# Kernel optimization log

Measured on AMD Instinct MI355X. Metric: run time of the kernel, lower is better.

Reference implementation:

```python
import jax, jax.numpy as jnp
import numpy as np

EMB = 384
H = 6
D = 64  # head_size = EMB // H
FF = 4 * EMB
B, T = 256, 256
EPS = 1e-5


def layernorm(x, g, b):
    mu = jnp.mean(x, axis=-1, keepdims=True)
    var = jnp.var(x, axis=-1, keepdims=True)
    return (x - mu) * jax.lax.rsqrt(var + EPS) * g + b


def setup_inputs() -> dict:
    key = jax.random.key(0)
    ks = jax.random.split(key, 12)
    s_qkv = 1.0 / np.sqrt(EMB)
    return {
        "x":  jax.random.normal(ks[0], (B, T, EMB), jnp.float32),
        # per-head Q/K/V projections stacked: [EMB, H, D]
        "Wq": jax.random.normal(ks[1], (EMB, H, D), jnp.float32) * s_qkv,
        "Wk": jax.random.normal(ks[2], (EMB, H, D), jnp.float32) * s_qkv,
        "Wv": jax.random.normal(ks[3], (EMB, H, D), jnp.float32) * s_qkv,
        "Wo": jax.random.normal(ks[4], (EMB, EMB), jnp.float32) * s_qkv,
        "bo": jnp.zeros((EMB,), jnp.float32),
        "W1": jax.random.normal(ks[5], (EMB, FF), jnp.float32) * s_qkv,
        "b1": jnp.zeros((FF,), jnp.float32),
        "W2": jax.random.normal(ks[6], (FF, EMB), jnp.float32) * (1.0 / np.sqrt(FF)),
        "b2": jnp.zeros((EMB,), jnp.float32),
        "g1": jnp.ones((EMB,), jnp.float32),
        "be1": jnp.zeros((EMB,), jnp.float32),
        "g2": jnp.ones((EMB,), jnp.float32),
        "be2": jnp.zeros((EMB,), jnp.float32),
    }


def reference(x, Wq, Wk, Wv, Wo, bo, W1, b1, W2, b2, g1, be1, g2, be2):
    # pre-LN attention (unmasked encoder block, dropout in eval mode = identity)
    h = layernorm(x, g1, be1)                      # [B,T,C]
    q = jnp.einsum('btc,chd->bhtd', h, Wq)
    k = jnp.einsum('btc,chd->bhtd', h, Wk)
    v = jnp.einsum('btc,chd->bhtd', h, Wv)
    scores = jnp.einsum('bhtd,bhsd->bhts', q, k) * (D ** -0.5)
    attn = jax.nn.softmax(scores, axis=-1)         # [B,H,T,T]
    o = jnp.einsum('bhts,bhsd->bhtd', attn, v)
    o = o.transpose(0, 2, 1, 3).reshape(x.shape[0], x.shape[1], EMB)  # concat heads
    x = x + o @ Wo + bo
    h2 = layernorm(x, g2, be2)
    ff = jax.nn.relu(h2 @ W1 + b1) @ W2 + b2
    return x + ff
```

## Files before the change

### kernel.cpp

```cpp
#include <hip/hip_runtime.h>

typedef __attribute__((ext_vector_type(8))) short bf16x8;
typedef __attribute__((ext_vector_type(4))) float f32x4;
typedef __attribute__((ext_vector_type(4))) unsigned short u16x4;

#define DEVFN static __device__ __forceinline__

DEVFN unsigned short f2b(float f) {
  union { float f; unsigned u; } x; x.f = f;
  unsigned r = x.u + 0x7FFFu + ((x.u >> 16) & 1u);
  return (unsigned short)(r >> 16);
}

DEVFN void gll16(const void* g, void* l) {
  __builtin_amdgcn_global_load_lds(
      (const __attribute__((address_space(1))) unsigned int*)g,
      (__attribute__((address_space(3))) unsigned int*)l, 16, 0, 0);
}

#define MFMA16(a, b, c) __builtin_amdgcn_mfma_f32_16x16x32_bf16((a), (b), (c), 0, 0, 0)

__global__ __launch_bounds__(256) void prep_kernel(
    const float* __restrict__ Wq, const float* __restrict__ Wk, const float* __restrict__ Wv,
    const float* __restrict__ Wo, const float* __restrict__ W1, const float* __restrict__ W2,
    short* __restrict__ wqkvT, short* __restrict__ woT,
    short* __restrict__ w1T, short* __restrict__ w2T)
{
  int idx = blockIdx.x * 256 + threadIdx.x;
  if (idx < 442368) {
    int n = idx / 384, kk = idx - n * 384;
    int sec = n / 384, ww = n - sec * 384;
    const float* s = sec == 0 ? Wq : (sec == 1 ? Wk : Wv);
    wqkvT[idx] = (short)f2b(s[kk * 384 + ww]);
  } else if (idx < 589824) {
    int j = idx - 442368;
    int n = j / 384, kk = j - n * 384;
    woT[j] = (short)f2b(Wo[kk * 384 + n]);
  } else if (idx < 1179648) {
    int j = idx - 589824;
    int n = j / 384, kk = j - n * 384;
    w1T[j] = (short)f2b(W1[kk * 1536 + n]);
  } else if (idx < 1769472) {
    int j = idx - 1179648;
    int n = j / 1536, kk = j - n * 1536;
    w2T[j] = (short)f2b(W2[kk * 384 + n]);
  }
}

__global__ __launch_bounds__(256) void ln_kernel(
    const float* __restrict__ x, const float* __restrict__ g, const float* __restrict__ b,
    short* __restrict__ out)
{
  int row = blockIdx.x * 4 + (threadIdx.x >> 6);
  int l = threadIdx.x & 63;
  const float* xr = x + (size_t)row * 384;
  float v[6], s = 0.f, s2 = 0.f;
  #pragma unroll
  for (int i = 0; i < 6; ++i) { v[i] = xr[l + 64 * i]; s += v[i]; s2 += v[i] * v[i]; }
  #pragma unroll
  for (int m = 1; m < 64; m <<= 1) { s += __shfl_xor(s, m); s2 += __shfl_xor(s2, m); }
  float mu = s * (1.f / 384.f);
  float rs = rsqrtf(s2 * (1.f / 384.f) - mu * mu + 1e-5f);
  short* orow = out + (size_t)row * 384;
  #pragma unroll
  for (int i = 0; i < 6; ++i) {
    int c = l + 64 * i;
    orow[c] = (short)f2b((v[i] - mu) * rs * g[c] + b[c]);
  }
}

template<int EPI>
__global__ __launch_bounds__(256) void gemm_bt(
    const short* __restrict__ A, const short* __restrict__ BT,
    int K, int kt, int N,
    const float* __restrict__ bias, const float* __restrict__ resid,
    float* __restrict__ fout, short* __restrict__ bout,
    short* __restrict__ qb, short* __restrict__ kb, short* __restrict__ vb)
{
  __shared__ short As[128 * 64];
  __shared__ short Bs[128 * 64];
  const int tid = threadIdx.x;
  const int l = tid & 63, w = tid >> 6;
  const int cl = l & 15, rq = l >> 4;
  const int wr = (w >> 1) * 64, wc = (w & 1) * 64;
  const int m0 = blockIdx.y * 128, n0 = blockIdx.x * 128;
  const short* Ab = A + (size_t)m0 * K;
  const short* Bb = BT + (size_t)n0 * K;

  f32x4 acc[4][4] = {};

  for (int ks = 0; ks < kt; ++ks) {
    const int k0 = ks * 64;
    __syncthreads();
    #pragma unroll
    for (int i = 0; i < 4; ++i) {
      int slot = i * 256 + tid;
      int row = slot >> 3, g = slot & 7;
      int gs = g ^ (row & 7);
      gll16(Ab + (size_t)row * K + k0 + gs * 8, &As[slot * 8]);
      gll16(Bb + (size_t)row * K + k0 + gs * 8, &Bs[slot * 8]);
    }
    __syncthreads();
    #pragma unroll
    for (int kk = 0; kk < 2; ++kk) {
      bf16x8 af[4], bfr[4];
      #pragma unroll
      for (int m = 0; m < 4; ++m) {
        int row = wr + m * 16 + cl;
        af[m] = *(const bf16x8*)&As[row * 64 + (((kk * 4 + rq) ^ (row & 7)) * 8)];
      }
      #pragma unroll
      for (int n = 0; n < 4; ++n) {
        int row = wc + n * 16 + cl;
        bfr[n] = *(const bf16x8*)&Bs[row * 64 + (((kk * 4 + rq) ^ (row & 7)) * 8)];
      }
      #pragma unroll
      for (int m = 0; m < 4; ++m)
        #pragma unroll
        for (int n = 0; n < 4; ++n)
          acc[m][n] = MFMA16(af[m], bfr[n], acc[m][n]);
    }
  }

  const int gr0 = m0 + wr, gc0 = n0 + wc;
  #pragma unroll
  for (int m = 0; m < 4; ++m) {
    #pragma unroll
    for (int n = 0; n < 4; ++n) {
      int col = gc0 + n * 16 + cl;
      int rbase = gr0 + m * 16 + rq * 4;
      if constexpr (EPI == 0) {
        int sec = col / 384;
        int wcol = col - sec * 384;
        int hh = wcol >> 6, d = wcol & 63;
        int bidx = rbase >> 8, t0 = rbase & 255;
        if (sec == 2) {
          u16x4 pk;
          #pragma unroll
          for (int r = 0; r < 4; ++r) pk[r] = f2b(acc[m][n][r]);
          *(u16x4*)&vb[((size_t)(bidx * 6 + hh) * 64 + d) * 256 + t0] = pk;
        } else {
          short* dst = (sec == 0) ? qb : kb;
          float sc = (sec == 0) ? 0.125f : 1.0f;
          #pragma unroll
          for (int r = 0; r < 4; ++r)
            dst[((size_t)(bidx * 6 + hh) * 256 + t0 + r) * 64 + d] = (short)f2b(acc[m][n][r] * sc);
        }
      } else if constexpr (EPI == 1) {
        #pragma unroll
        for (int r = 0; r < 4; ++r) {
          size_t ix = (size_t)(rbase + r) * N + col;
          fout[ix] = acc[m][n][r] + bias[col] + resid[ix];
        }
      } else {
        #pragma unroll
        for (int r = 0; r < 4; ++r)
          bout[(size_t)(rbase + r) * N + col] = (short)f2b(fmaxf(acc[m][n][r] + bias[col], 0.f));
      }
    }
  }
}

__global__ __launch_bounds__(256) void attn_kernel(
    const short* __restrict__ qg, const short* __restrict__ kg,
    const short* __restrict__ vg, short* __restrict__ og)
{
  __shared__ short Ks[256 * 64];
  __shared__ short Vs[64 * 256];
  __shared__ float Pb[4][16 * 36];
  const int tid = threadIdx.x;
  const int bh = blockIdx.x >> 2;
  const int q0 = (blockIdx.x & 3) * 64;
  const int w = tid >> 6, l = tid & 63;
  const int cl = l & 15, rq = l >> 4;
  const short* kgb = kg + (size_t)bh * 16384;
  const short* vgb = vg + (size_t)bh * 16384;
  #pragma unroll
  for (int i = 0; i < 8; ++i) {
    int slot = i * 256 + tid;
    int row = slot >> 3, g = slot & 7;
    gll16(kgb + row * 64 + (g ^ (row & 7)) * 8, &Ks[slot * 8]);
  }
  #pragma unroll
  for (int i = 0; i < 8; ++i) {
    int slot = i * 256 + tid;
    int row = slot >> 5, g = slot & 31;
    int gs = (g & 24) | ((g ^ row) & 7);
    gll16(vgb + row * 256 + gs * 8, &Vs[slot * 8]);
  }
  const int qrow = q0 + w * 16 + cl;
  const bf16x8* qp = (const bf16x8*)(qg + ((size_t)bh * 256 + qrow) * 64 + rq * 8);
  bf16x8 qf0 = qp[0];
  bf16x8 qf1 = qp[4];
  __syncthreads();

  f32x4 s[16] = {};
  #pragma unroll
  for (int c = 0; c < 16; ++c) {
    int scol = c * 16 + cl;
    bf16x8 b0 = *(const bf16x8*)&Ks[scol * 64 + ((rq ^ (scol & 7)) * 8)];
    bf16x8 b1 = *(const bf16x8*)&Ks[scol * 64 + (((4 + rq) ^ (scol & 7)) * 8)];
    s[c] = MFMA16(qf0, b0, s[c]);
    s[c] = MFMA16(qf1, b1, s[c]);
  }
  float mx[4], inv[4];
  #pragma unroll
  for (int r = 0; r < 4; ++r) {
    float m = s[0][r];
    #pragma unroll
    for (int c = 1; c < 16; ++c) m = fmaxf(m, s[c][r]);
    #pragma unroll
    for (int msk = 1; msk < 16; msk <<= 1) m = fmaxf(m, __shfl_xor(m, msk));
    mx[r] = m;
  }
  #pragma unroll
  for (int r = 0; r < 4; ++r) {
    float t = 0.f;
    #pragma unroll
    for (int c = 0; c < 16; ++c) { float e = __expf(s[c][r] - mx[r]); s[c][r] = e; t += e; }
    #pragma unroll
    for (int msk = 1; msk < 16; msk <<= 1) t += __shfl_xor(t, msk);
    inv[r] = 1.f / t;
  }
  #pragma unroll
  for (int c = 0; c < 16; ++c) {
    #pragma unroll
    for (int r = 0; r < 4; ++r) s[c][r] *= inv[r];
  }
  f32x4 oacc[4] = {};
  float* Pw = Pb[w];
  #pragma unroll
  for (int ch = 0; ch < 8; ++ch) {
    #pragma unroll
    for (int r = 0; r < 4; ++r) {
      Pw[(4 * rq + r) * 36 + cl]      = s[2 * ch][r];
      Pw[(4 * rq + r) * 36 + 16 + cl] = s[2 * ch + 1][r];
    }
    f32x4 lo = *(const f32x4*)&Pw[cl * 36 + rq * 8];
    f32x4 hi = *(const f32x4*)&Pw[cl * 36 + rq * 8 + 4];
    bf16x8 pa;
    #pragma unroll
    for (int j = 0; j < 4; ++j) { pa[j] = (short)f2b(lo[j]); pa[j + 4] = (short)f2b(hi[j]); }
    #pragma unroll
    for (int n = 0; n < 4; ++n) {
      int vrow = n * 16 + cl;
      int gg = ch * 4 + rq;
      int gs = (gg & 24) | ((gg ^ vrow) & 7);
      bf16x8 vf = *(const bf16x8*)&Vs[vrow * 256 + gs * 8];
      oacc[n] = MFMA16(pa, vf, oacc[n]);
    }
  }
  int b = bh / 6, hh = bh - b * 6;
  #pragma unroll
  for (int n = 0; n < 4; ++n) {
    #pragma unroll
    for (int r = 0; r < 4; ++r) {
      int trow = q0 + w * 16 + 4 * rq + r;
      og[((size_t)(b * 256 + trow)) * 384 + hh * 64 + n * 16 + cl] = (short)f2b(oacc[n][r]);
    }
  }
}

extern "C" void kernel_launch(void* const* d_in, const int* in_sizes, int n_in,
                              void* d_out, int out_size, void* d_ws, size_t ws_size,
                              hipStream_t stream) {
  const float* x   = (const float*)d_in[0];
  const float* Wq  = (const float*)d_in[1];
  const float* Wk  = (const float*)d_in[2];
  const float* Wv  = (const float*)d_in[3];
  const float* Wo  = (const float*)d_in[4];
  const float* bo  = (const float*)d_in[5];
  const float* W1  = (const float*)d_in[6];
  const float* b1  = (const float*)d_in[7];
  const float* W2  = (const float*)d_in[8];
  const float* b2  = (const float*)d_in[9];
  const float* g1  = (const float*)d_in[10];
  const float* be1 = (const float*)d_in[11];
  const float* g2  = (const float*)d_in[12];
  const float* be2 = (const float*)d_in[13];

  char* ws = (char*)d_ws;
  short* wqkvT = (short*)(ws);
  short* woT   = (short*)(ws + 884736);
  short* w1T   = (short*)(ws + 1179648);
  short* w2T   = (short*)(ws + 2359296);
  short* bufA  = (short*)(ws + 3538944);
  short* h  = bufA;
  short* q  = bufA + 25165824;
  short* k  = bufA + 50331648;
  short* v  = bufA + 75497472;
  short* o  = bufA;
  float* x2 = (float*)(bufA + 25165824);
  short* h2 = bufA + 75497472;
  short* act = bufA;
  float* out = (float*)d_out;

  prep_kernel<<<6912, 256, 0, stream>>>(Wq, Wk, Wv, Wo, W1, W2, wqkvT, woT, w1T, w2T);
  ln_kernel<<<16384, 256, 0, stream>>>(x, g1, be1, h);
  gemm_bt<0><<<dim3(9, 512), 256, 0, stream>>>(h, wqkvT, 384, 6, 1152,
      nullptr, nullptr, nullptr, nullptr, q, k, v);
  attn_kernel<<<6144, 256, 0, stream>>>(q, k, v, o);
  gemm_bt<1><<<dim3(3, 512), 256, 0, stream>>>(o, woT, 384, 6, 384,
      bo, x, x2, nullptr, nullptr, nullptr, nullptr);
  ln_kernel<<<16384, 256, 0, stream>>>(x2, g2, be2, h2);
  for (int c = 0; c < 4; ++c) {
    const size_t roff = (size_t)c * 16384 * 384;
    gemm_bt<2><<<dim3(12, 128), 256, 0, stream>>>(h2 + roff, w1T, 384, 6, 1536,
        b1, nullptr, nullptr, act, nullptr, nullptr, nullptr);
    gemm_bt<1><<<dim3(3, 128), 256, 0, stream>>>(act, w2T, 1536, 24, 384,
        b2, x2 + roff, out + roff, nullptr, nullptr, nullptr, nullptr);
  }
}
```

Baseline: 633.8 us.

## Enlarge GEMM tiles to 256x128 with 512 threads and XCD-aware block remap

The bf16 GEMM now uses 512-thread blocks computing 256x128 output tiles, which halves the B-tile reloads per output row. It also uses a 1-D grid with a remap that keeps neighbouring tiles on the same XCD, to improve L2 reuse. The residual stream is now written directly into the output buffer and the FFN residual is updated in place. The FFN is processed in 2 chunks instead of 4, giving larger launches. The larger tiles use more LDS and registers per block, which may reduce occupancy.

```diff
diff --git a/kernel.cpp b/kernel.cpp
--- a/kernel.cpp
+++ b/kernel.cpp
@@ -70,20 +70,27 @@
 }
 
 template<int EPI>
-__global__ __launch_bounds__(256) void gemm_bt(
+__global__ __launch_bounds__(512) void gemm_bt(
     const short* __restrict__ A, const short* __restrict__ BT,
-    int K, int kt, int N,
+    int K, int kt, int N, int nx,
     const float* __restrict__ bias, const float* __restrict__ resid,
     float* __restrict__ fout, short* __restrict__ bout,
     short* __restrict__ qb, short* __restrict__ kb, short* __restrict__ vb)
 {
-  __shared__ short As[128 * 64];
+  __shared__ short As[256 * 64];
   __shared__ short Bs[128 * 64];
   const int tid = threadIdx.x;
   const int l = tid & 63, w = tid >> 6;
   const int cl = l & 15, rq = l >> 4;
   const int wr = (w >> 1) * 64, wc = (w & 1) * 64;
-  const int m0 = blockIdx.y * 128, n0 = blockIdx.x * 128;
+
+  const int nwg = gridDim.x, bid = blockIdx.x;
+  const int q8 = nwg >> 3, r8 = nwg & 7;
+  const int xcd = bid & 7, ii = bid >> 3;
+  const int wg = (xcd < r8) ? xcd * (q8 + 1) + ii : r8 * (q8 + 1) + (xcd - r8) * q8 + ii;
+  const int bx = wg % nx, by = wg / nx;
+
+  const int m0 = by * 256, n0 = bx * 128;
   const short* Ab = A + (size_t)m0 * K;
   const short* Bb = BT + (size_t)n0 * K;
 
@@ -94,10 +101,16 @@
     __syncthreads();
     #pragma unroll
     for (int i = 0; i < 4; ++i) {
-      int slot = i * 256 + tid;
+      int slot = i * 512 + tid;
       int row = slot >> 3, g = slot & 7;
       int gs = g ^ (row & 7);
       gll16(Ab + (size_t)row * K + k0 + gs * 8, &As[slot * 8]);
+    }
+    #pragma unroll
+    for (int i = 0; i < 2; ++i) {
+      int slot = i * 512 + tid;
+      int row = slot >> 3, g = slot & 7;
+      int gs = g ^ (row & 7);
       gll16(Bb + (size_t)row * K + k0 + gs * 8, &Bs[slot * 8]);
     }
     __syncthreads();
@@ -290,24 +303,24 @@
   short* k  = bufA + 50331648;
   short* v  = bufA + 75497472;
   short* o  = bufA;
-  float* x2 = (float*)(bufA + 25165824);
-  short* h2 = bufA + 75497472;
-  short* act = bufA;
+  short* h2 = bufA + 25165824;
+  short* act = bufA + 50331648;
   float* out = (float*)d_out;
 
   prep_kernel<<<6912, 256, 0, stream>>>(Wq, Wk, Wv, Wo, W1, W2, wqkvT, woT, w1T, w2T);
   ln_kernel<<<16384, 256, 0, stream>>>(x, g1, be1, h);
-  gemm_bt<0><<<dim3(9, 512), 256, 0, stream>>>(h, wqkvT, 384, 6, 1152,
+  gemm_bt<0><<<9 * 256, 512, 0, stream>>>(h, wqkvT, 384, 6, 1152, 9,
       nullptr, nullptr, nullptr, nullptr, q, k, v);
   attn_kernel<<<6144, 256, 0, stream>>>(q, k, v, o);
-  gemm_bt<1><<<dim3(3, 512), 256, 0, stream>>>(o, woT, 384, 6, 384,
-      bo, x, x2, nullptr, nullptr, nullptr, nullptr);
-  ln_kernel<<<16384, 256, 0, stream>>>(x2, g2, be2, h2);
-  for (int c = 0; c < 4; ++c) {
-    const size_t roff = (size_t)c * 16384 * 384;
-    gemm_bt<2><<<dim3(12, 128), 256, 0, stream>>>(h2 + roff, w1T, 384, 6, 1536,
+  gemm_bt<1><<<3 * 256, 512, 0, stream>>>(o, woT, 384, 6, 384, 3,
+      bo, x, out, nullptr, nullptr, nullptr, nullptr);
+  ln_kernel<<<16384, 256, 0, stream>>>(out, g2, be2, h2);
+  for (int c = 0; c < 2; ++c) {
+    const size_t roff = (size_t)c * 32768 * 384;
+    const size_t ooff = (size_t)c * 32768 * 384;
+    gemm_bt<2><<<12 * 128, 512, 0, stream>>>(h2 + roff, w1T, 384, 6, 1536, 12,
         b1, nullptr, nullptr, act, nullptr, nullptr, nullptr);
-    gemm_bt<1><<<dim3(3, 128), 256, 0, stream>>>(act, w2T, 1536, 24, 384,
-        b2, x2 + roff, out + roff, nullptr, nullptr, nullptr, nullptr);
-  }
-}
+    gemm_bt<1><<<3 * 128, 512, 0, stream>>>(act, w2T, 1536, 24, 384, 3,
+        b2, out + ooff, out + ooff, nullptr, nullptr, nullptr, nullptr);
+  }
+}
```

Measured after the change: 528.9 us (median of 2 runs). -16.6%, faster.
